# Optimization experiments

Measured on AMD Instinct MI355X. Metric: run time of the kernel, lower is better.

Reference implementation:

```python
import jax, jax.numpy as jnp
import numpy as np
import math

B, S, D, H, DFF, L = 8, 1024, 512, 8, 2048, 4
DK = D // H
EPS = 1e-5
NEG = -1e32


def _sinusoidal_pe(s, d):
    pos = np.arange(s)[:, None].astype(np.float32)
    div = np.exp(np.arange(0, d, 2).astype(np.float32) * (-math.log(10000.0) / d))
    pe = np.zeros((s, d), np.float32)
    pe[:, 0::2] = np.sin(pos * div)
    pe[:, 1::2] = np.cos(pos * div)
    return jnp.asarray(pe)


def setup_inputs() -> dict:
    key = jax.random.key(0)
    ks = jax.random.split(key, 20)
    sd = 0.02
    inp = {
        "q_embed_data": jax.random.normal(ks[0], (B, S, D), jnp.float32),
        "qa_embed_data": jax.random.normal(ks[1], (B, S, D), jnp.float32),
        "pe": _sinusoidal_pe(S, D),
        # stacked per-layer params (leading dim L). kq_same=1 -> q uses Wk.
        "Wk": sd * jax.random.normal(ks[2], (L, D, D), jnp.float32),
        "bk": jnp.zeros((L, D), jnp.float32),
        "Wv": sd * jax.random.normal(ks[3], (L, D, D), jnp.float32),
        "bv": jnp.zeros((L, D), jnp.float32),
        "Wo": sd * jax.random.normal(ks[4], (L, D, D), jnp.float32),
        "bo": jnp.zeros((L, D), jnp.float32),
        "ln1_s": jnp.ones((L, D), jnp.float32),
        "ln1_b": jnp.zeros((L, D), jnp.float32),
        "W1": sd * jax.random.normal(ks[5], (L, D, DFF), jnp.float32),
        "b1": jnp.zeros((L, DFF), jnp.float32),
        "W2": sd * jax.random.normal(ks[6], (L, DFF, D), jnp.float32),
        "b2": jnp.zeros((L, D), jnp.float32),
        "ln2_s": jnp.ones((L, D), jnp.float32),
        "ln2_b": jnp.zeros((L, D), jnp.float32),
    }
    return inp


def _layernorm(z, s, b):
    m = z.mean(-1, keepdims=True)
    v = ((z - m) ** 2).mean(-1, keepdims=True)
    return (z - m) / jnp.sqrt(v + EPS) * s + b


def _forward(q_embed_data, qa_embed_data, pe, Wk, bk, Wv, bv, Wo, bo,
             ln1_s, ln1_b, W1, b1, W2, b2, ln2_s, ln2_b):
    x = q_embed_data + pe[None, :, :]
    y = qa_embed_data + pe[None, :, :]  # values source stays fixed across blocks
    allowed = jnp.tril(jnp.ones((S, S), bool), -1)  # strictly-causal: attend only to j < i
    row_keep = (jnp.arange(S) > 0).astype(x.dtype)[None, None, :, None]  # zero_pad row 0

    def heads(z, W, b):
        return (z @ W + b).reshape(B, S, H, DK).transpose(0, 2, 1, 3)  # [B,H,S,DK]

    def step(xc, p):
        wk, bk_, wv, bv_, wo, bo_, s1, b1n, w1, b1f, w2, b2f, s2, b2n = p
        q = heads(xc, wk, bk_)  # kq_same: q via k_linear
        k = heads(xc, wk, bk_)
        v = heads(y, wv, bv_)
        sc = jnp.einsum('bhid,bhjd->bhij', q, k) / math.sqrt(DK)
        att = jax.nn.softmax(jnp.where(allowed, sc, NEG), axis=-1) * row_keep
        o = jnp.einsum('bhij,bhjd->bhid', att, v).transpose(0, 2, 1, 3).reshape(B, S, D)
        x1 = _layernorm(xc + (o @ wo + bo_), s1, b1n)
        f = jax.nn.relu(x1 @ w1 + b1f) @ w2 + b2f
        x2 = _layernorm(x1 + f, s2, b2n)
        return x2, None

    out, _ = jax.lax.scan(step, x, (Wk, bk, Wv, bv, Wo, bo, ln1_s, ln1_b, W1, b1, W2, b2, ln2_s, ln2_b))
    return out


def reference(q_embed_data, qa_embed_data, pe, Wk, bk, Wv, bv, Wo, bo,
              ln1_s, ln1_b, W1, b1, W2, b2, ln2_s, ln2_b):
    return _forward(q_embed_data, qa_embed_data, pe, Wk, bk, Wv, bv, Wo, bo,
                    ln1_s, ln1_b, W1, b1, W2, b2, ln2_s, ln2_b)
```

## Files before the change

kernel.cpp:

```cpp
#include <hip/hip_runtime.h>
#include <stdint.h>

typedef __attribute__((ext_vector_type(8))) __bf16 bf16x8;
typedef __attribute__((ext_vector_type(4))) float f32x4;
typedef __attribute__((ext_vector_type(4))) unsigned int u32x4;

constexpr int B = 8, S = 1024, D = 512, H = 8, DFF = 2048, L = 4, DK = 64;
constexpr int MR = B * S;

__device__ __forceinline__ unsigned short f2bf(float f) {
    union { float f; unsigned u; } v; v.f = f;
    unsigned u = v.u;
    u += 0x7fffu + ((u >> 16) & 1u);
    return (unsigned short)(u >> 16);
}

__device__ __forceinline__ void gload_lds16(const void* g, void* l) {
    __builtin_amdgcn_global_load_lds(
        (const __attribute__((address_space(1))) void*)g,
        (__attribute__((address_space(3))) void*)l, 16, 0, 0);
}

__global__ __launch_bounds__(256) void add_pe_kernel(
    const float* __restrict__ qe, const float* __restrict__ qa,
    const float* __restrict__ pe, float* __restrict__ x_f32,
    unsigned short* __restrict__ x_bf, unsigned short* __restrict__ y_bf) {
    int gid = blockIdx.x * 256 + threadIdx.x;
    int base = gid * 4;
    int po = base & (S * D - 1);
    float4 p = *(const float4*)(pe + po);
    float4 a = *(const float4*)(qe + base);
    float4 q = *(const float4*)(qa + base);
    float4 xv = make_float4(a.x + p.x, a.y + p.y, a.z + p.z, a.w + p.w);
    float4 yv = make_float4(q.x + p.x, q.y + p.y, q.z + p.z, q.w + p.w);
    *(float4*)(x_f32 + base) = xv;
    ushort4 xb; xb.x = f2bf(xv.x); xb.y = f2bf(xv.y); xb.z = f2bf(xv.z); xb.w = f2bf(xv.w);
    ushort4 yb; yb.x = f2bf(yv.x); yb.y = f2bf(yv.y); yb.z = f2bf(yv.z); yb.w = f2bf(yv.w);
    *(ushort4*)(x_bf + base) = xb;
    *(ushort4*)(y_bf + base) = yb;
}

__global__ __launch_bounds__(256) void wtrans_kernel(
    const float* __restrict__ src, unsigned short* __restrict__ dst, int K, int N) {
    __shared__ float t[64][65];
    src += (size_t)blockIdx.z * K * N;
    dst += (size_t)blockIdx.z * K * N;
    int n0 = blockIdx.x * 64, k0 = blockIdx.y * 64;
    int tid = threadIdx.x;
    int r = tid >> 4, c4 = (tid & 15) * 4;
    #pragma unroll
    for (int rr = 0; rr < 64; rr += 16) {
        float4 v = *(const float4*)(src + (size_t)(k0 + r + rr) * N + n0 + c4);
        t[r + rr][c4] = v.x; t[r + rr][c4 + 1] = v.y;
        t[r + rr][c4 + 2] = v.z; t[r + rr][c4 + 3] = v.w;
    }
    __syncthreads();
    int n = tid >> 2, kc = (tid & 3) * 16;
    ushort4 o[4];
    #pragma unroll
    for (int g = 0; g < 4; g++) {
        o[g].x = f2bf(t[kc + g * 4 + 0][n]);
        o[g].y = f2bf(t[kc + g * 4 + 1][n]);
        o[g].z = f2bf(t[kc + g * 4 + 2][n]);
        o[g].w = f2bf(t[kc + g * 4 + 3][n]);
    }
    unsigned short* dp = dst + (size_t)(n0 + n) * K + k0 + kc;
    #pragma unroll
    for (int g = 0; g < 4; g++) *(ushort4*)(dp + g * 4) = o[g];
}

template<int BN, bool RELU, bool RESID, bool OUT_F32, bool OUT_BF16, bool OUT_VT>
__global__ __launch_bounds__(256) void gemm_kernel(
    const unsigned short* __restrict__ A, const unsigned short* __restrict__ Bt,
    const float* __restrict__ bias, const float* __restrict__ resid,
    float* __restrict__ out_f32, unsigned short* __restrict__ out_bf,
    int M, int N, int K) {
    constexpr int MT = (BN == 128) ? 4 : 2;
    constexpr int WROWS = (BN == 128) ? 64 : 32;
    constexpr int BRND = (BN == 128) ? 4 : 2;
    __shared__ unsigned short a_lds[128 * 64];
    __shared__ unsigned short b_lds[BN * 64];

    const int tid = threadIdx.x;
    const int lane = tid & 63, wid = tid >> 6;
    const int wm = (BN == 128) ? (wid >> 1) : wid;
    const int wn = (BN == 128) ? (wid & 1) : 0;
    const int l15 = lane & 15, quad = lane >> 4;
    const int m0 = blockIdx.x * 128, n0 = blockIdx.y * BN;

    f32x4 acc[MT][4];
    #pragma unroll
    for (int i = 0; i < MT; i++)
        #pragma unroll
        for (int j = 0; j < 4; j++) { f32x4 z = {0.f, 0.f, 0.f, 0.f}; acc[i][j] = z; }

    const unsigned short* aP[4];
    unsigned short* aL[4];
    #pragma unroll
    for (int j = 0; j < 4; j++) {
        int c = wid * 256 + j * 64 + lane;
        int r = c >> 3, slot = c & 7, kg = slot ^ (r & 7);
        aP[j] = A + (size_t)(m0 + r) * K + kg * 8;
        aL[j] = a_lds + (size_t)(wid * 256 + j * 64) * 8;
    }
    const unsigned short* bP[BRND];
    unsigned short* bL[BRND];
    #pragma unroll
    for (int j = 0; j < BRND; j++) {
        int c = wid * (BRND * 64) + j * 64 + lane;
        int r = c >> 3, slot = c & 7, kg = slot ^ (r & 7);
        bP[j] = Bt + (size_t)(n0 + r) * K + kg * 8;
        bL[j] = b_lds + (size_t)(wid * (BRND * 64) + j * 64) * 8;
    }

    for (int k0 = 0; k0 < K; k0 += 64) {
        #pragma unroll
        for (int j = 0; j < 4; j++) gload_lds16(aP[j] + k0, aL[j]);
        #pragma unroll
        for (int j = 0; j < BRND; j++) gload_lds16(bP[j] + k0, bL[j]);
        __syncthreads();

        bf16x8 af[MT][2], bfv[4][2];
        #pragma unroll
        for (int mt = 0; mt < MT; mt++) {
            int row = wm * WROWS + mt * 16 + l15;
            #pragma unroll
            for (int kh = 0; kh < 2; kh++)
                af[mt][kh] = *(const bf16x8*)&a_lds[row * 64 + (((kh * 4 + quad) ^ (row & 7)) * 8)];
        }
        #pragma unroll
        for (int nt = 0; nt < 4; nt++) {
            int row = wn * 64 + nt * 16 + l15;
            #pragma unroll
            for (int kh = 0; kh < 2; kh++)
                bfv[nt][kh] = *(const bf16x8*)&b_lds[row * 64 + (((kh * 4 + quad) ^ (row & 7)) * 8)];
        }
        #pragma unroll
        for (int mt = 0; mt < MT; mt++)
            #pragma unroll
            for (int nt = 0; nt < 4; nt++) {
                acc[mt][nt] = __builtin_amdgcn_mfma_f32_16x16x32_bf16(af[mt][0], bfv[nt][0], acc[mt][nt], 0, 0, 0);
                acc[mt][nt] = __builtin_amdgcn_mfma_f32_16x16x32_bf16(af[mt][1], bfv[nt][1], acc[mt][nt], 0, 0, 0);
            }
        __syncthreads();
    }

    #pragma unroll
    for (int nt = 0; nt < 4; nt++) {
        int col = n0 + wn * 64 + nt * 16 + l15;
        float bv = bias[col];
        #pragma unroll
        for (int mt = 0; mt < MT; mt++) {
            int row0 = m0 + wm * WROWS + mt * 16 + quad * 4;
            if (OUT_VT) {
                int hh = col >> 6, d = col & 63;
                int bb = row0 >> 10, s0 = row0 & 1023;
                ushort4 o;
                o.x = f2bf(acc[mt][nt][0] + bv);
                o.y = f2bf(acc[mt][nt][1] + bv);
                o.z = f2bf(acc[mt][nt][2] + bv);
                o.w = f2bf(acc[mt][nt][3] + bv);
                *(ushort4*)(out_bf + ((size_t)(bb * H + hh) * DK + d) * S + s0) = o;
            } else {
                #pragma unroll
                for (int r = 0; r < 4; r++) {
                    int row = row0 + r;
                    float v = acc[mt][nt][r] + bv;
                    if (RESID) v += resid[(size_t)row * N + col];
                    if (RELU) v = fmaxf(v, 0.f);
                    size_t o = (size_t)row * N + col;
                    if (OUT_F32) out_f32[o] = v;
                    if (OUT_BF16) out_bf[o] = f2bf(v);
                }
            }
        }
    }
}

__global__ __launch_bounds__(256) void ln_kernel(
    const float* __restrict__ in, const float* __restrict__ gamma,
    const float* __restrict__ beta, float* __restrict__ out_f32,
    unsigned short* __restrict__ out_bf) {
    __shared__ float red[8];
    int row = blockIdx.x, tid = threadIdx.x;
    const float* p = in + (size_t)row * D;
    float2 v = *(const float2*)(p + tid * 2);
    float s = v.x + v.y;
    float q = v.x * v.x + v.y * v.y;
    #pragma unroll
    for (int off = 32; off > 0; off >>= 1) {
        s += __shfl_xor(s, off);
        q += __shfl_xor(q, off);
    }
    int wid = tid >> 6, lane = tid & 63;
    if (lane == 0) { red[wid] = s; red[4 + wid] = q; }
    __syncthreads();
    s = red[0] + red[1] + red[2] + red[3];
    q = red[4] + red[5] + red[6] + red[7];
    float mean = s * (1.f / D);
    float var = q * (1.f / D) - mean * mean;
    float inv = rsqrtf(var + 1e-5f);
    int c = tid * 2;
    float2 g = *(const float2*)(gamma + c);
    float2 bb = *(const float2*)(beta + c);
    float o0 = (v.x - mean) * inv * g.x + bb.x;
    float o1 = (v.y - mean) * inv * g.y + bb.y;
    *(float2*)(out_f32 + (size_t)row * D + c) = make_float2(o0, o1);
    ushort2 ob; ob.x = f2bf(o0); ob.y = f2bf(o1);
    *(ushort2*)(out_bf + (size_t)row * D + c) = ob;
}

__device__ __forceinline__ void load_kfrag(const unsigned short* kbase, int kt,
                                           int l15, int quad, bf16x8 (&kf)[4][2]) {
    #pragma unroll
    for (int mt = 0; mt < 4; mt++) {
        const unsigned short* kr = kbase + (size_t)(kt * 64 + mt * 16 + l15) * D;
        kf[mt][0] = *(const bf16x8*)(kr + quad * 8);
        kf[mt][1] = *(const bf16x8*)(kr + 32 + quad * 8);
    }
}
__device__ __forceinline__ void load_vfrag(const unsigned short* vbase, int kt,
                                           int l15, int quad, bf16x8 (&vf)[4][2]) {
    #pragma unroll
    for (int mt = 0; mt < 4; mt++) {
        const unsigned short* vr = vbase + (size_t)(mt * 16 + l15) * S + kt * 64;
        vf[mt][0] = *(const bf16x8*)(vr + quad * 8);
        vf[mt][1] = *(const bf16x8*)(vr + 32 + quad * 8);
    }
}

__global__ __launch_bounds__(64, 2) void attn_part_kernel(
    const unsigned short* __restrict__ qk, const unsigned short* __restrict__ vt,
    float* __restrict__ part_o, float* __restrict__ part_l) {
    __shared__ unsigned p_u32[32 * 36];
    constexpr float C = 0.18033688011112042f;
    const float NEGINF = -__builtin_huge_valf();

    int bx = blockIdx.x;
    int slot = 47 - (bx >> 6);
    int head = bx & 63;
    int b = head >> 3, h = head & 7;
    int lane = threadIdx.x;
    int l15 = lane & 15, quad = lane >> 4;

    int t, ck0, ck1;
    if (slot < 16)      { t = slot;      ck0 = 0;       ck1 = (t >> 1) + 1; }
    else if (slot < 32) { t = slot;      int nt = (t >> 1) + 1; ck0 = 0;       ck1 = nt >> 1; }
    else                { t = slot - 16; int nt = (t >> 1) + 1; ck0 = nt >> 1; ck1 = nt; }

    const int rowbase = b * S, colbase = h * DK;
    const unsigned short* kbase = qk + (size_t)rowbase * D + colbase;
    const unsigned short* vbase = vt + (size_t)(b * H + h) * (DK * S);

    bf16x8 qf[2][2];
    #pragma unroll
    for (int u = 0; u < 2; u++) {
        const unsigned short* qrow =
            qk + (size_t)(rowbase + t * 32 + u * 16 + l15) * D + colbase;
        qf[u][0] = *(const bf16x8*)(qrow + quad * 8);
        qf[u][1] = *(const bf16x8*)(qrow + 32 + quad * 8);
    }

    float l_r[2] = {0.f, 0.f};
    f32x4 o_acc[2][4];
    #pragma unroll
    for (int u = 0; u < 2; u++)
        #pragma unroll
        for (int i = 0; i < 4; i++) { f32x4 z = {0.f, 0.f, 0.f, 0.f}; o_acc[u][i] = z; }

    auto process = [&](int kt, bf16x8 (&kf)[4][2], bf16x8 (&vf)[4][2], bool diag) {
        f32x4 s[2][4];
        #pragma unroll
        for (int u = 0; u < 2; u++) {
            const int qb = t * 32 + u * 16;
            #pragma unroll
            for (int mt = 0; mt < 4; mt++) {
                if (!diag || (kt * 64 + mt * 16 < qb + 16)) {
                    f32x4 a = {0.f, 0.f, 0.f, 0.f};
                    a = __builtin_amdgcn_mfma_f32_16x16x32_bf16(kf[mt][0], qf[u][0], a, 0, 0, 0);
                    a = __builtin_amdgcn_mfma_f32_16x16x32_bf16(kf[mt][1], qf[u][1], a, 0, 0, 0);
                    s[u][mt] = a;
                } else {
                    f32x4 a = {NEGINF, NEGINF, NEGINF, NEGINF};
                    s[u][mt] = a;
                }
            }
        }
        if (diag) {
            #pragma unroll
            for (int u = 0; u < 2; u++) {
                const int gi = t * 32 + u * 16 + l15;
                #pragma unroll
                for (int mt = 0; mt < 4; mt++)
                    #pragma unroll
                    for (int r = 0; r < 4; r++) {
                        int gj = kt * 64 + mt * 16 + quad * 4 + r;
                        s[u][mt][r] = (gj >= gi) ? NEGINF : s[u][mt][r];
                    }
            }
        }
        #pragma unroll
        for (int u = 0; u < 2; u++) {
            const int ql = u * 16 + l15;
            #pragma unroll
            for (int mt = 0; mt < 4; mt++) {
                unsigned a0 = __builtin_bit_cast(unsigned, exp2f(s[u][mt][0] * C));
                unsigned a1 = __builtin_bit_cast(unsigned, exp2f(s[u][mt][1] * C));
                unsigned a2 = __builtin_bit_cast(unsigned, exp2f(s[u][mt][2] * C));
                unsigned a3 = __builtin_bit_cast(unsigned, exp2f(s[u][mt][3] * C));
                p_u32[ql * 36 + mt * 8 + quad * 2]     = (a0 >> 16) | (a1 & 0xffff0000u);
                p_u32[ql * 36 + mt * 8 + quad * 2 + 1] = (a2 >> 16) | (a3 & 0xffff0000u);
                float q0 = __builtin_bit_cast(float, a0 & 0xffff0000u);
                float q1 = __builtin_bit_cast(float, a1 & 0xffff0000u);
                float q2 = __builtin_bit_cast(float, a2 & 0xffff0000u);
                float q3 = __builtin_bit_cast(float, a3 & 0xffff0000u);
                l_r[u] += (q0 + q1) + (q2 + q3);
            }
        }
        bf16x8 pb[2][2];
        #pragma unroll
        for (int u = 0; u < 2; u++) {
            const int ql = u * 16 + l15;
            u32x4 d0 = *(const u32x4*)&p_u32[ql * 36 + quad * 4];
            u32x4 d1 = *(const u32x4*)&p_u32[ql * 36 + 16 + quad * 4];
            pb[u][0] = __builtin_bit_cast(bf16x8, d0);
            pb[u][1] = __builtin_bit_cast(bf16x8, d1);
        }
        #pragma unroll
        for (int u = 0; u < 2; u++)
            #pragma unroll
            for (int mt = 0; mt < 4; mt++) {
                o_acc[u][mt] = __builtin_amdgcn_mfma_f32_16x16x32_bf16(vf[mt][0], pb[u][0], o_acc[u][mt], 0, 0, 0);
                o_acc[u][mt] = __builtin_amdgcn_mfma_f32_16x16x32_bf16(vf[mt][1], pb[u][1], o_acc[u][mt], 0, 0, 0);
            }
    };

    bf16x8 ka[4][2], kb[4][2], va[4][2];
    load_kfrag(kbase, ck0, l15, quad, ka);
    int kt = ck0;
    while (true) {
        load_vfrag(vbase, kt, l15, quad, va);
        if (kt + 1 < ck1) load_kfrag(kbase, kt + 1, l15, quad, kb);
        process(kt, ka, va, 2 * kt + 2 > t);
        if (++kt >= ck1) break;
        load_vfrag(vbase, kt, l15, quad, va);
        if (kt + 1 < ck1) load_kfrag(kbase, kt + 1, l15, quad, ka);
        process(kt, kb, va, 2 * kt + 2 > t);
        if (++kt >= ck1) break;
    }

    #pragma unroll
    for (int u = 0; u < 2; u++) {
        l_r[u] += __shfl_xor(l_r[u], 16);
        l_r[u] += __shfl_xor(l_r[u], 32);
    }

    int p = head * 48 + slot;
    if (quad == 0) {
        #pragma unroll
        for (int u = 0; u < 2; u++)
            part_l[(size_t)p * 32 + u * 16 + l15] = l_r[u];
    }
    float* po = part_o + (size_t)p * 2048;
    #pragma unroll
    for (int u = 0; u < 2; u++)
        #pragma unroll
        for (int mt = 0; mt < 4; mt++)
            #pragma unroll
            for (int r = 0; r < 4; r++)
                po[(mt * 16 + quad * 4 + r) * 32 + u * 16 + l15] = o_acc[u][mt][r];
}

__global__ __launch_bounds__(256) void attn_combine_kernel(
    const float* __restrict__ part_o, const float* __restrict__ part_l,
    unsigned short* __restrict__ ob) {
    int bx = blockIdx.x;
    int t = bx & 31, head = bx >> 5;
    int b = head >> 3, h = head & 7;
    int tid = threadIdx.x;
    int q = tid >> 3, dg = (tid & 7) * 8;
    int p0 = head * 48 + t;
    bool two = (t >= 16);
    int p1 = head * 48 + t + 16;

    float ldenom = part_l[(size_t)p0 * 32 + q];
    if (two) ldenom += part_l[(size_t)p1 * 32 + q];
    float inv = (ldenom > 0.f) ? 1.f / ldenom : 0.f;
    int si = t * 32 + q;
    if (si == 0) inv = 0.f;

    const float* po0 = part_o + (size_t)p0 * 2048;
    const float* po1 = part_o + (size_t)p1 * 2048;
    unsigned short out[8];
    #pragma unroll
    for (int i = 0; i < 8; i++) {
        int d = dg + i;
        float v = po0[d * 32 + q];
        if (two) v += po1[d * 32 + q];
        out[i] = f2bf(v * inv);
    }
    unsigned short* dst = ob + (size_t)(b * S + si) * D + h * DK + dg;
    *(u32x4*)dst = *(const u32x4*)out;
}

extern "C" void kernel_launch(void* const* d_in, const int* in_sizes, int n_in,
                              void* d_out, int out_size, void* d_ws, size_t ws_size,
                              hipStream_t stream) {
    (void)in_sizes; (void)n_in; (void)out_size; (void)ws_size;
    const float* qe  = (const float*)d_in[0];
    const float* qa  = (const float*)d_in[1];
    const float* pe  = (const float*)d_in[2];
    const float* Wk  = (const float*)d_in[3];
    const float* bk  = (const float*)d_in[4];
    const float* Wv  = (const float*)d_in[5];
    const float* bv  = (const float*)d_in[6];
    const float* Wo  = (const float*)d_in[7];
    const float* bo  = (const float*)d_in[8];
    const float* l1s = (const float*)d_in[9];
    const float* l1b = (const float*)d_in[10];
    const float* W1  = (const float*)d_in[11];
    const float* b1  = (const float*)d_in[12];
    const float* W2  = (const float*)d_in[13];
    const float* b2  = (const float*)d_in[14];
    const float* l2s = (const float*)d_in[15];
    const float* l2b = (const float*)d_in[16];

    char* w = (char*)d_ws;
    float* x_f32  = (float*)w;           w += (size_t)MR * D * 4;
    float* t_f32  = (float*)w;           w += (size_t)MR * D * 4;
    float* x1_f32 = (float*)w;           w += (size_t)MR * D * 4;
    unsigned short* x_bf  = (unsigned short*)w; w += (size_t)MR * D * 2;
    unsigned short* y_bf  = (unsigned short*)w; w += (size_t)MR * D * 2;
    unsigned short* qk_bf = (unsigned short*)w; w += (size_t)MR * D * 2;
    unsigned short* vt_bf = (unsigned short*)w; w += (size_t)MR * D * 2;
    unsigned short* o_bf  = (unsigned short*)w; w += (size_t)MR * D * 2;
    unsigned short* x1_bf = (unsigned short*)w; w += (size_t)MR * D * 2;
    unsigned short* h_bf  = (unsigned short*)w; w += (size_t)MR * DFF * 2;
    unsigned short* wkT = (unsigned short*)w;   w += (size_t)L * D * D * 2;
    unsigned short* wvT = (unsigned short*)w;   w += (size_t)L * D * D * 2;
    unsigned short* woT = (unsigned short*)w;   w += (size_t)L * D * D * 2;
    unsigned short* w1T = (unsigned short*)w;   w += (size_t)L * D * DFF * 2;
    unsigned short* w2T = (unsigned short*)w;   w += (size_t)L * DFF * D * 2;
    float* part_o = (float*)w;                  w += (size_t)3072 * 2048 * 4;
    float* part_l = (float*)w;                  w += (size_t)3072 * 32 * 4;

    add_pe_kernel<<<MR * D / 4 / 256, 256, 0, stream>>>(qe, qa, pe, x_f32, x_bf, y_bf);
    wtrans_kernel<<<dim3(8, 8, L), 256, 0, stream>>>(Wk, wkT, D, D);
    wtrans_kernel<<<dim3(8, 8, L), 256, 0, stream>>>(Wv, wvT, D, D);
    wtrans_kernel<<<dim3(8, 8, L), 256, 0, stream>>>(Wo, woT, D, D);
    wtrans_kernel<<<dim3(32, 8, L), 256, 0, stream>>>(W1, w1T, D, DFF);
    wtrans_kernel<<<dim3(8, 32, L), 256, 0, stream>>>(W2, w2T, DFF, D);

    dim3 g512(64, 8), g2048(64, 16);
    for (int l = 0; l < L; l++) {
        gemm_kernel<64, false, false, false, true, false><<<g512, 256, 0, stream>>>(
            x_bf, wkT + (size_t)l * D * D, bk + l * D, nullptr, nullptr, qk_bf, MR, D, D);
        gemm_kernel<64, false, false, false, false, true><<<g512, 256, 0, stream>>>(
            y_bf, wvT + (size_t)l * D * D, bv + l * D, nullptr, nullptr, vt_bf, MR, D, D);
        attn_part_kernel<<<48 * 64, 64, 0, stream>>>(qk_bf, vt_bf, part_o, part_l);
        attn_combine_kernel<<<64 * 32, 256, 0, stream>>>(part_o, part_l, o_bf);
        gemm_kernel<64, false, true, true, false, false><<<g512, 256, 0, stream>>>(
            o_bf, woT + (size_t)l * D * D, bo + l * D, x_f32, t_f32, nullptr, MR, D, D);
        ln_kernel<<<MR, 256, 0, stream>>>(t_f32, l1s + l * D, l1b + l * D, x1_f32, x1_bf);
        gemm_kernel<128, true, false, false, true, false><<<g2048, 256, 0, stream>>>(
            x1_bf, w1T + (size_t)l * D * DFF, b1 + l * DFF, nullptr, nullptr, h_bf, MR, DFF, D);
        gemm_kernel<64, false, true, true, false, false><<<g512, 256, 0, stream>>>(
            h_bf, w2T + (size_t)l * DFF * D, b2 + l * D, x1_f32, t_f32, nullptr, MR, D, DFF);
        float* xo = (l == L - 1) ? (float*)d_out : x_f32;
        ln_kernel<<<MR, 256, 0, stream>>>(t_f32, l2s + l * D, l2b + l * D, xo, x_bf);
    }
}
```

Baseline: 826.6 us.

## Remap GEMM tiles per XCD and streamline causal attention softmax path

The GEMM block index is remapped so that contiguous M-tiles are grouped onto the same XCD, which is meant to improve L2 reuse of A rows. The attention kernel raises occupancy to 4 waves per SIMD and double-buffers the P tile in LDS. It also fuses masking, exp, hardware bf16 packing and the row sum per tile, and skips masked MFMAs in the PV product on diagonal blocks. Head-to-block mapping is reordered so consecutive blocks hit different batches, and the partial outputs now use nontemporal stores and loads. The row sum changes from bf16-rounded values to full fp32 values, which slightly alters numerics, and the higher occupancy target risks register spills.

```diff
diff --git a/kernel.cpp b/kernel.cpp
--- a/kernel.cpp
+++ b/kernel.cpp
@@ -86,7 +86,12 @@
     const int wm = (BN == 128) ? (wid >> 1) : wid;
     const int wn = (BN == 128) ? (wid & 1) : 0;
     const int l15 = lane & 15, quad = lane >> 4;
-    const int m0 = blockIdx.x * 128, n0 = blockIdx.y * BN;
+    const int nmt = gridDim.x, nnt = gridDim.y;
+    const int o_lin = blockIdx.y * nmt + blockIdx.x;
+    const int xcd = o_lin & 7, oi = o_lin >> 3;
+    const int mtile = xcd * (nmt >> 3) + oi / nnt;
+    const int ntile = oi % nnt;
+    const int m0 = mtile * 128, n0 = ntile * BN;
 
     f32x4 acc[MT][4];
     #pragma unroll
@@ -229,17 +234,18 @@
     }
 }
 
-__global__ __launch_bounds__(64, 2) void attn_part_kernel(
+__global__ __launch_bounds__(64, 4) void attn_part_kernel(
     const unsigned short* __restrict__ qk, const unsigned short* __restrict__ vt,
     float* __restrict__ part_o, float* __restrict__ part_l) {
-    __shared__ unsigned p_u32[32 * 36];
+    __shared__ unsigned p_u32[2][32 * 36];
     constexpr float C = 0.18033688011112042f;
     const float NEGINF = -__builtin_huge_valf();
 
     int bx = blockIdx.x;
     int slot = 47 - (bx >> 6);
-    int head = bx & 63;
-    int b = head >> 3, h = head & 7;
+    int hh = bx & 63;
+    int b = hh & 7, h = hh >> 3;
+    int head = b * 8 + h;
     int lane = threadIdx.x;
     int l15 = lane & 15, quad = lane >> 4;
 
@@ -250,7 +256,7 @@
 
     const int rowbase = b * S, colbase = h * DK;
     const unsigned short* kbase = qk + (size_t)rowbase * D + colbase;
-    const unsigned short* vbase = vt + (size_t)(b * H + h) * (DK * S);
+    const unsigned short* vbase = vt + (size_t)head * (DK * S);
 
     bf16x8 qf[2][2];
     #pragma unroll
@@ -268,71 +274,60 @@
         #pragma unroll
         for (int i = 0; i < 4; i++) { f32x4 z = {0.f, 0.f, 0.f, 0.f}; o_acc[u][i] = z; }
 
-    auto process = [&](int kt, bf16x8 (&kf)[4][2], bf16x8 (&vf)[4][2], bool diag) {
-        f32x4 s[2][4];
+    auto process = [&](int kt, bf16x8 (&kf)[4][2], bf16x8 (&vf)[4][2], int par) {
+        const bool diag = 2 * kt + 2 > t;
+        unsigned* pb = p_u32[par];
         #pragma unroll
         for (int u = 0; u < 2; u++) {
             const int qb = t * 32 + u * 16;
+            const int ql = u * 16 + l15;
             #pragma unroll
             for (int mt = 0; mt < 4; mt++) {
                 if (!diag || (kt * 64 + mt * 16 < qb + 16)) {
                     f32x4 a = {0.f, 0.f, 0.f, 0.f};
                     a = __builtin_amdgcn_mfma_f32_16x16x32_bf16(kf[mt][0], qf[u][0], a, 0, 0, 0);
                     a = __builtin_amdgcn_mfma_f32_16x16x32_bf16(kf[mt][1], qf[u][1], a, 0, 0, 0);
-                    s[u][mt] = a;
+                    if (diag) {
+                        const int gi = qb + l15;
+                        #pragma unroll
+                        for (int r = 0; r < 4; r++) {
+                            int gj = kt * 64 + mt * 16 + quad * 4 + r;
+                            a[r] = (gj >= gi) ? NEGINF : a[r];
+                        }
+                    }
+                    float e0 = exp2f(a[0] * C), e1 = exp2f(a[1] * C);
+                    float e2 = exp2f(a[2] * C), e3 = exp2f(a[3] * C);
+                    unsigned pk0, pk1;
+                    asm("v_cvt_pk_bf16_f32 %0, %1, %2" : "=v"(pk0) : "v"(e0), "v"(e1));
+                    asm("v_cvt_pk_bf16_f32 %0, %1, %2" : "=v"(pk1) : "v"(e2), "v"(e3));
+                    l_r[u] += (e0 + e1) + (e2 + e3);
+                    *(uint2*)&pb[ql * 36 + mt * 8 + quad * 2] = make_uint2(pk0, pk1);
                 } else {
-                    f32x4 a = {NEGINF, NEGINF, NEGINF, NEGINF};
-                    s[u][mt] = a;
+                    *(uint2*)&pb[ql * 36 + mt * 8 + quad * 2] = make_uint2(0u, 0u);
                 }
             }
         }
-        if (diag) {
-            #pragma unroll
-            for (int u = 0; u < 2; u++) {
-                const int gi = t * 32 + u * 16 + l15;
+        #pragma unroll
+        for (int u = 0; u < 2; u++) {
+            const int qb = t * 32 + u * 16;
+            const int ql = u * 16 + l15;
+            u32x4 d0 = *(const u32x4*)&pb[ql * 36 + quad * 4];
+            bf16x8 pb0 = __builtin_bit_cast(bf16x8, d0);
+            const bool hi = (kt * 64 + 32 < qb + 16);
+            if (hi) {
+                u32x4 d1 = *(const u32x4*)&pb[ql * 36 + 16 + quad * 4];
+                bf16x8 pb1 = __builtin_bit_cast(bf16x8, d1);
+                #pragma unroll
+                for (int mt = 0; mt < 4; mt++) {
+                    o_acc[u][mt] = __builtin_amdgcn_mfma_f32_16x16x32_bf16(vf[mt][0], pb0, o_acc[u][mt], 0, 0, 0);
+                    o_acc[u][mt] = __builtin_amdgcn_mfma_f32_16x16x32_bf16(vf[mt][1], pb1, o_acc[u][mt], 0, 0, 0);
+                }
+            } else {
                 #pragma unroll
                 for (int mt = 0; mt < 4; mt++)
-                    #pragma unroll
-                    for (int r = 0; r < 4; r++) {
-                        int gj = kt * 64 + mt * 16 + quad * 4 + r;
-                        s[u][mt][r] = (gj >= gi) ? NEGINF : s[u][mt][r];
-                    }
+                    o_acc[u][mt] = __builtin_amdgcn_mfma_f32_16x16x32_bf16(vf[mt][0], pb0, o_acc[u][mt], 0, 0, 0);
             }
         }
-        #pragma unroll
-        for (int u = 0; u < 2; u++) {
-            const int ql = u * 16 + l15;
-            #pragma unroll
-            for (int mt = 0; mt < 4; mt++) {
-                unsigned a0 = __builtin_bit_cast(unsigned, exp2f(s[u][mt][0] * C));
-                unsigned a1 = __builtin_bit_cast(unsigned, exp2f(s[u][mt][1] * C));
-                unsigned a2 = __builtin_bit_cast(unsigned, exp2f(s[u][mt][2] * C));
-                unsigned a3 = __builtin_bit_cast(unsigned, exp2f(s[u][mt][3] * C));
-                p_u32[ql * 36 + mt * 8 + quad * 2]     = (a0 >> 16) | (a1 & 0xffff0000u);
-                p_u32[ql * 36 + mt * 8 + quad * 2 + 1] = (a2 >> 16) | (a3 & 0xffff0000u);
-                float q0 = __builtin_bit_cast(float, a0 & 0xffff0000u);
-                float q1 = __builtin_bit_cast(float, a1 & 0xffff0000u);
-                float q2 = __builtin_bit_cast(float, a2 & 0xffff0000u);
-                float q3 = __builtin_bit_cast(float, a3 & 0xffff0000u);
-                l_r[u] += (q0 + q1) + (q2 + q3);
-            }
-        }
-        bf16x8 pb[2][2];
-        #pragma unroll
-        for (int u = 0; u < 2; u++) {
-            const int ql = u * 16 + l15;
-            u32x4 d0 = *(const u32x4*)&p_u32[ql * 36 + quad * 4];
-            u32x4 d1 = *(const u32x4*)&p_u32[ql * 36 + 16 + quad * 4];
-            pb[u][0] = __builtin_bit_cast(bf16x8, d0);
-            pb[u][1] = __builtin_bit_cast(bf16x8, d1);
-        }
-        #pragma unroll
-        for (int u = 0; u < 2; u++)
-            #pragma unroll
-            for (int mt = 0; mt < 4; mt++) {
-                o_acc[u][mt] = __builtin_amdgcn_mfma_f32_16x16x32_bf16(vf[mt][0], pb[u][0], o_acc[u][mt], 0, 0, 0);
-                o_acc[u][mt] = __builtin_amdgcn_mfma_f32_16x16x32_bf16(vf[mt][1], pb[u][1], o_acc[u][mt], 0, 0, 0);
-            }
     };
 
     bf16x8 ka[4][2], kb[4][2], va[4][2];
@@ -341,11 +336,11 @@
     while (true) {
         load_vfrag(vbase, kt, l15, quad, va);
         if (kt + 1 < ck1) load_kfrag(kbase, kt + 1, l15, quad, kb);
-        process(kt, ka, va, 2 * kt + 2 > t);
+        process(kt, ka, va, 0);
         if (++kt >= ck1) break;
         load_vfrag(vbase, kt, l15, quad, va);
         if (kt + 1 < ck1) load_kfrag(kbase, kt + 1, l15, quad, ka);
-        process(kt, kb, va, 2 * kt + 2 > t);
+        process(kt, kb, va, 1);
         if (++kt >= ck1) break;
     }
 
@@ -359,7 +354,7 @@
     if (quad == 0) {
         #pragma unroll
         for (int u = 0; u < 2; u++)
-            part_l[(size_t)p * 32 + u * 16 + l15] = l_r[u];
+            __builtin_nontemporal_store(l_r[u], &part_l[(size_t)p * 32 + u * 16 + l15]);
     }
     float* po = part_o + (size_t)p * 2048;
     #pragma unroll
@@ -368,7 +363,8 @@
         for (int mt = 0; mt < 4; mt++)
             #pragma unroll
             for (int r = 0; r < 4; r++)
-                po[(mt * 16 + quad * 4 + r) * 32 + u * 16 + l15] = o_acc[u][mt][r];
+                __builtin_nontemporal_store(o_acc[u][mt][r],
+                    &po[(mt * 16 + quad * 4 + r) * 32 + u * 16 + l15]);
 }
 
 __global__ __launch_bounds__(256) void attn_combine_kernel(
@@ -383,8 +379,8 @@
     bool two = (t >= 16);
     int p1 = head * 48 + t + 16;
 
-    float ldenom = part_l[(size_t)p0 * 32 + q];
-    if (two) ldenom += part_l[(size_t)p1 * 32 + q];
+    float ldenom = __builtin_nontemporal_load(&part_l[(size_t)p0 * 32 + q]);
+    if (two) ldenom += __builtin_nontemporal_load(&part_l[(size_t)p1 * 32 + q]);
     float inv = (ldenom > 0.f) ? 1.f / ldenom : 0.f;
     int si = t * 32 + q;
     if (si == 0) inv = 0.f;
@@ -395,8 +391,8 @@
     #pragma unroll
     for (int i = 0; i < 8; i++) {
         int d = dg + i;
-        float v = po0[d * 32 + q];
-        if (two) v += po1[d * 32 + q];
+        float v = __builtin_nontemporal_load(&po0[d * 32 + q]);
+        if (two) v += __builtin_nontemporal_load(&po1[d * 32 + q]);
         out[i] = f2bf(v * inv);
     }
     unsigned short* dst = ob + (size_t)(b * S + si) * D + h * DK + dg;
```

Result: slower. 1.074 ms (+30.0%).
